# Performance work log

Hardware: AMD Instinct MI355X
Metric: run time of the kernel (lower is better)

Reference implementation:

```python
import jax, jax.numpy as jnp
import numpy as np

KSIZE, SCALE, STRIDE, SOFTMAX_SCALE = 3, 3, 1, 10.0
ESCAPE_NAN = 1e-4
DN = ('NCHW', 'OIHW', 'NCHW')


def same_pad(x, k, stride):
    # torch same_padding: pad so out = ceil(in/stride)
    H, W = x.shape[-2], x.shape[-1]
    oh, ow = -(-H // stride), -(-W // stride)
    ph = max(0, (oh - 1) * stride + k - H)
    pw = max(0, (ow - 1) * stride + k - W)
    return jnp.pad(x, ((0, 0), (0, 0), (ph // 2, ph - ph // 2), (pw // 2, pw - pw // 2)))


def extract_patches(img, k, stride):
    # img [B,C,H,W] already padded -> [B, L, C, k, k], matching torch Unfold ordering (C slowest, kh, kw)
    B, C, H, W = img.shape
    oh, ow = (H - k) // stride + 1, (W - k) // stride + 1
    cols = [img[:, :, i:i + stride * oh:stride, j:j + stride * ow:stride]
            for i in range(k) for j in range(k)]
    p = jnp.stack(cols, axis=2)                      # [B, C, k*k, oh, ow]
    p = p.reshape(B, C, k, k, oh * ow)               # [B, C, k, k, L]
    return jnp.transpose(p, (0, 4, 1, 2, 3))         # [B, L, C, k, k]


def conv1x1_prelu(x, W, b, a):
    y = jnp.einsum('bchw,oc->bohw', x, W) + b[None, :, None, None]
    return jnp.where(y >= 0, y, a * y)


def bilinear_down(x, Ho, Wo):
    # F.interpolate(mode='bilinear', align_corners=False), no antialias
    H, W = x.shape[-2], x.shape[-1]
    def coords(o, s):
        src = (jnp.arange(o, dtype=jnp.float32) + 0.5) * (s / o) - 0.5
        src = jnp.clip(src, 0.0, s - 1.0)
        i0 = jnp.floor(src).astype(jnp.int32)
        i1 = jnp.minimum(i0 + 1, s - 1)
        return i0, i1, src - i0.astype(jnp.float32)
    y0, y1, wy = coords(Ho, H)
    x0, x1, wx = coords(Wo, W)
    r = x[:, :, y0, :] * (1.0 - wy)[:, None] + x[:, :, y1, :] * wy[:, None]
    return r[:, :, :, x0] * (1.0 - wx) + r[:, :, :, x1] * wx


def forward(x, Wa, ba, aa, Wm1, bm1, am1, Wm2, bm2, am2):
    B, C, H, W = x.shape
    kernel = SCALE * KSIZE  # 9
    embed_w = conv1x1_prelu(x, Wa, ba, aa)      # [B,C,H,W]
    match = conv1x1_prelu(x, Wm1, bm1, am1)     # [B,C/2,H,W]
    # large-scale patches used as conv_transpose kernels: [B, L, C, 9, 9]
    raw_w = extract_patches(same_pad(embed_w, kernel, STRIDE * SCALE), kernel, STRIDE * SCALE)
    Hr, Wr = H // SCALE, W // SCALE
    ref = conv1x1_prelu(bilinear_down(x, Hr, Wr), Wm2, bm2, am2)  # [B,C/2,Hr,Wr]
    # small-scale patches used as correlation kernels: [B, L, C/2, 3, 3]
    w = extract_patches(same_pad(ref, KSIZE, STRIDE), KSIZE, STRIDE)
    norm = jnp.sqrt(jnp.sum(w * w, axis=(2, 3, 4), keepdims=True))
    wn = w / jnp.maximum(norm, ESCAPE_NAN)
    xp = same_pad(match, KSIZE, 1)  # [B,C/2,H+2,W+2]

    def corr(xi, wi):  # xi [C/2,H+2,W+2], wi [L,C/2,3,3] -> [L,H,W]
        return jax.lax.conv_general_dilated(xi[None], wi, (1, 1), 'VALID', dimension_numbers=DN)[0]

    y = jax.vmap(corr)(xp, wn)                  # [B,L,H,W]
    y = jax.nn.softmax(y * SOFTMAX_SCALE, axis=1)

    pad = kernel - 1 - SCALE  # conv_transpose2d(stride=3, padding=3) equivalent padding = 5

    def tconv(yi, rwi):  # yi [L,H,W], rwi [L,C,9,9] -> [C,3H,3W]
        k = jnp.transpose(jnp.flip(rwi, (-2, -1)), (1, 0, 2, 3))  # [C,L,9,9]
        return jax.lax.conv_general_dilated(
            yi[None], k, (1, 1), [(pad, pad), (pad, pad)],
            lhs_dilation=(STRIDE * SCALE, STRIDE * SCALE), dimension_numbers=DN)[0]

    out = jax.vmap(tconv)(y, raw_w) / 6.0       # [B,C,3H,3W]
    return out


def setup_inputs() -> dict:
    key = jax.random.key(0)
    ks = jax.random.split(key, 8)
    B, C, H, W = 4, 64, 60, 60
    C2 = C // 2
    return {
        'x': jax.random.normal(ks[0], (B, C, H, W), jnp.float32),
        'Wa': jax.random.normal(ks[1], (C, C), jnp.float32) * 0.1,
        'ba': jax.random.normal(ks[2], (C,), jnp.float32) * 0.1,
        'aa': jnp.full((1,), 0.25, jnp.float32),
        'Wm1': jax.random.normal(ks[3], (C2, C), jnp.float32) * 0.1,
        'bm1': jax.random.normal(ks[4], (C2,), jnp.float32) * 0.1,
        'am1': jnp.full((1,), 0.25, jnp.float32),
        'Wm2': jax.random.normal(ks[5], (C2, C), jnp.float32) * 0.1,
        'bm2': jax.random.normal(ks[6], (C2,), jnp.float32) * 0.1,
        'am2': jnp.full((1,), 0.25, jnp.float32),
    }


def reference(x, Wa, ba, aa, Wm1, bm1, am1, Wm2, bm2, am2):
    return forward(x, Wa, ba, aa, Wm1, bm1, am1, Wm2, bm2, am2)
```

## Files before the change

### kernel.cpp

```cpp
#include <hip/hip_runtime.h>
#include <hip/hip_bf16.h>

typedef __hip_bfloat16 bf16_t;
using f32x4  = __attribute__((ext_vector_type(4))) float;
using bf16x8 = __attribute__((ext_vector_type(8))) short;

#define NB 4
#define NC 64
#define NC2 32
#define NH 60
#define NW 60
#define NPIX (NH*NW)
#define HP 66
#define MP 62
#define HR 20
#define RP 22
#define NL 400
#define OHW 180
#define KPAD 512

#define OFF_XPB   2230272
#define OFF_REFP  3214336
#define OFF_YBL   3462144
#define OFF_AP    14982144
#define OFF_EB    29727744
#define OFF_XP    32087040
#define OFF_RF    40381440

__global__ __launch_bounds__(256) void k_conv(
    const float* __restrict__ x,
    const float* __restrict__ Wa,  const float* __restrict__ ba,  const float* __restrict__ aa,
    const float* __restrict__ Wm1, const float* __restrict__ bm1, const float* __restrict__ am1,
    const float* __restrict__ Wm2, const float* __restrict__ bm2, const float* __restrict__ am2,
    bf16_t* __restrict__ E_bt, bf16_t* __restrict__ xpb, float* __restrict__ refp) {
  int bid = blockIdx.x;
  int t = threadIdx.x;
  if (bid < 300) {
    __shared__ float Ws[64*64];
    __shared__ float bs[64];
    __shared__ float al;
    int b = bid / 75, pblk = bid % 75;
    for (int i = t; i < 64*64; i += 256) {
      int co = i >> 6, c = i & 63;
      Ws[c*64 + co] = Wa[i];
    }
    if (t < 64) bs[t] = ba[t];
    if (t == 0) al = aa[0];
    __syncthreads();
    int lane = t & 63, wid = t >> 6;
    int pix0 = pblk*48 + wid*12;
    const float* xb = x + b*NC*NPIX + pix0;
    float acc[12];
    #pragma unroll
    for (int p = 0; p < 12; ++p) acc[p] = bs[lane];
    for (int c = 0; c < 64; ++c) {
      float wv = Ws[c*64 + lane];
      const float* xc = xb + c*NPIX;
      #pragma unroll
      for (int p = 0; p < 12; ++p)
        acc[p] = fmaf(xc[p], wv, acc[p]);
    }
    #pragma unroll
    for (int p = 0; p < 12; ++p) {
      float v = acc[p];
      v = v >= 0.f ? v : al*v;
      int pix = pix0 + p;
      int ph = pix / NW, pw = pix % NW;
      E_bt[((b*HP + ph+3)*HP + (pw+3))*NC + lane] = __float2bfloat16(v);
    }
  } else if (bid < 2100) {
    int idx = (bid - 300)*256 + t;
    int pix = idx % NPIX; int tmp = idx / NPIX;
    int co = tmp % NC2; int b = tmp / NC2;
    float alpha = am1[0];
    const float* xb = x + b*NC*NPIX + pix;
    const float* wr = Wm1 + co*64;
    float acc = bm1[co];
    #pragma unroll 8
    for (int c = 0; c < 64; ++c)
      acc = fmaf(xb[c*NPIX], wr[c], acc);
    acc = acc >= 0.f ? acc : alpha*acc;
    int ph = pix / NW, pw = pix % NW;
    xpb[((b*NC2 + co)*MP + ph+1)*MP + (pw+1)] = __float2bfloat16(acc);
  } else {
    int idx = (bid - 2100)*256 + t;
    int pos = idx % (HR*HR); int tmp = idx / (HR*HR);
    int co = tmp % NC2; int b = tmp / NC2;
    int hr = pos / HR, wr_ = pos % HR;
    float alpha = am2[0];
    const float* xb = x + b*NC*NPIX + (3*hr+1)*NW + (3*wr_+1);
    const float* wrow = Wm2 + co*64;
    float acc = bm2[co];
    #pragma unroll 8
    for (int c = 0; c < 64; ++c)
      acc = fmaf(xb[c*NPIX], wrow[c], acc);
    acc = acc >= 0.f ? acc : alpha*acc;
    refp[((b*NC2 + co)*RP + hr+1)*RP + (wr_+1)] = acc;
  }
}

__global__ __launch_bounds__(256) void k_swz(
    const bf16_t* __restrict__ xpb, const float* __restrict__ refp,
    const bf16_t* __restrict__ E_bt,
    bf16_t* __restrict__ Xp, bf16_t* __restrict__ Rf, bf16_t* __restrict__ Eb) {
  __shared__ float scl[16];
  int bid = blockIdx.x;
  int t = threadIdx.x;
  if (bid < 2025) {
    int tid = bid*256 + t;
    int slot = tid & 63; int rest = tid >> 6;
    int ks = rest % 9; int rest2 = rest / 9;
    int mblk = rest2 % 225; int b = rest2 / 225;
    int m = mblk*16 + (slot & 15);
    int h = m / NW, w = m % NW;
    int k0 = ks*32 + (slot >> 4)*8;
    const bf16_t* xb = xpb + (size_t)b*NC2*MP*MP;
    union { bf16_t a[8]; bf16x8 v; } u;
    #pragma unroll
    for (int j = 0; j < 8; ++j) {
      int k = k0 + j;
      int c = k / 9, r = k % 9;
      int i = r / 3, j2 = r % 3;
      u.a[j] = xb[(c*MP + h + i)*MP + w + j2];
    }
    *(bf16x8*)(Xp + (size_t)tid*8) = u.v;
  } else if (bid < 2125) {
    int r2 = bid - 2025;
    int nblk = r2 % 25, b = r2 / 25;
    int ll = t >> 4, sub = t & 15;
    int l = nblk*16 + ll;
    int lh = l / HR, lw = l % HR;
    const float* rb = refp + (size_t)b*NC2*RP*RP;
    float ss = 0.f;
    #pragma unroll
    for (int e0 = 0; e0 < 18; ++e0) {
      int e = sub*18 + e0;
      int c = e / 9, r = e % 9;
      int i = r / 3, j = r % 3;
      float v = rb[(c*RP + lh + i)*RP + lw + j];
      ss = fmaf(v, v, ss);
    }
    #pragma unroll
    for (int off = 1; off < 16; off <<= 1)
      ss += __shfl_xor(ss, off);
    if (sub == 0) scl[ll] = 10.f / fmaxf(sqrtf(ss), 1e-4f);
    __syncthreads();
    for (int sidx = t; sidx < 576; sidx += 256) {
      int ks = sidx >> 6, slot = sidx & 63;
      int l2 = nblk*16 + (slot & 15);
      int lh2 = l2 / HR, lw2 = l2 % HR;
      float sc = scl[slot & 15];
      int k0 = ks*32 + (slot >> 4)*8;
      union { bf16_t a[8]; bf16x8 v; } u;
      #pragma unroll
      for (int j = 0; j < 8; ++j) {
        int k = k0 + j;
        int c = k / 9, r = k % 9;
        int i = r / 3, j2 = r % 3;
        u.a[j] = __float2bfloat16(rb[(c*RP + lh2 + i)*RP + lw2 + j2] * sc);
      }
      *(bf16x8*)(Rf + ((size_t)(b*25 + nblk)*576 + sidx)*8) = u.v;
    }
  } else {
    int r2 = bid - 2125;
    int n = r2 % 576, b = r2 / 576;
    int c = n / 9, n9 = n % 9, rr = n9 / 3, s = n9 % 3;
    size_t nbase = ((size_t)(b*12 + n/48)*16);
    const unsigned short* Eu = (const unsigned short*)E_bt;
    unsigned short* Ebu = (unsigned short*)Eb;
    for (int k = t; k < KPAD; k += 256) {
      unsigned short v = 0;
      if (k < 484) {
        int u = k / 22, vv = k % 22;
        v = Eu[((size_t)((b*HP + 3*u + rr)*HP + 3*vv + s))*NC + c];
      }
      size_t idx = (((nbase + (k>>5))*3 + (n%48)/16)*64 + ((k>>3)&3)*16 + (n&15))*8 + (k&7);
      Ebu[idx] = v;
    }
  }
}

__global__ __launch_bounds__(64) void k_cgemm(
    const bf16x8* __restrict__ Xp, const bf16x8* __restrict__ Rf,
    bf16_t* __restrict__ y_bl) {
  __shared__ __align__(16) bf16_t ytile[48][80];
  int L = threadIdx.x;
  int o = blockIdx.x;
  int xcd = o & 7, sl = o >> 3;
  int w = (xcd < 4 ? xcd*188 : 752 + (xcd-4)*187) + sl;
  int b = w / 375; int rem = w % 375;
  int mt = rem / 5, nt = rem % 5;
  const bf16x8* pa = Xp + ((size_t)(b*225 + mt*3)*9)*64 + L;
  const bf16x8* pb = Rf + ((size_t)(b*25 + nt*5)*9)*64 + L;
  f32x4 acc[3][5];
  #pragma unroll
  for (int i = 0; i < 3; ++i)
    #pragma unroll
    for (int j = 0; j < 5; ++j)
      acc[i][j] = {0.f, 0.f, 0.f, 0.f};
  bf16x8 af[3], bf[5], afn[3], bfn[5];
  #pragma unroll
  for (int i = 0; i < 3; ++i) af[i] = pa[i*576];
  #pragma unroll
  for (int j = 0; j < 5; ++j) bf[j] = pb[j*576];
  for (int ks = 0; ks < 9; ++ks) {
    if (ks < 8) {
      #pragma unroll
      for (int i = 0; i < 3; ++i) afn[i] = pa[i*576 + (ks+1)*64];
      #pragma unroll
      for (int j = 0; j < 5; ++j) bfn[j] = pb[j*576 + (ks+1)*64];
    }
    #pragma unroll
    for (int i = 0; i < 3; ++i)
      #pragma unroll
      for (int j = 0; j < 5; ++j)
        acc[i][j] = __builtin_amdgcn_mfma_f32_16x16x32_bf16(af[i], bf[j], acc[i][j], 0, 0, 0);
    #pragma unroll
    for (int i = 0; i < 3; ++i) af[i] = afn[i];
    #pragma unroll
    for (int j = 0; j < 5; ++j) bf[j] = bfn[j];
  }
  int quad = L >> 4, col = L & 15;
  #pragma unroll
  for (int mf = 0; mf < 3; ++mf)
    #pragma unroll
    for (int r = 0; r < 4; ++r)
      #pragma unroll
      for (int nf = 0; nf < 5; ++nf)
        ytile[mf*16 + quad*4 + r][nf*16 + col] = __float2bfloat16(acc[mf][nf][r]);
  __syncthreads();
  bf16_t* dst0 = y_bl + ((size_t)(b*NPIX + mt*48))*NL + nt*80;
  for (int i = L; i < 480; i += 64) {
    int row = i / 10, seg = i % 10;
    *(bf16x8*)(dst0 + (size_t)row*NL + seg*8) = *(const bf16x8*)&ytile[row][seg*8];
  }
}

__device__ __forceinline__ float lo_bf(unsigned int u) {
  return __uint_as_float(u << 16);
}
__device__ __forceinline__ float hi_bf(unsigned int u) {
  return __uint_as_float(u & 0xffff0000u);
}
__device__ __forceinline__ float u16_bf(unsigned short u) {
  return __uint_as_float(((unsigned int)u) << 16);
}
__device__ __forceinline__ unsigned short bf_bits(float f) {
  union { bf16_t h; unsigned short u; } c;
  c.h = __float2bfloat16(f);
  return c.u;
}

__global__ __launch_bounds__(512) void k_saprime(
    const unsigned int* __restrict__ y_b32, bf16_t* __restrict__ Ap) {
  __shared__ uint4 raw[2592];
  unsigned short* ysp = (unsigned short*)raw;
  int t = threadIdx.x;
  int b = blockIdx.z;
  int h0base = blockIdx.y*4, w0base = blockIdx.x*4;
  for (int i = t; i < 2592; i += 512) raw[i] = uint4{0,0,0,0};
  __syncthreads();

  int wave = t >> 6, lane = t & 63;
  bool act = lane < 50;
  for (int pos = wave; pos < 36; pos += 8) {
    int i = pos / 6, jj = pos % 6;
    int hh = h0base - 1 + i, ww = w0base - 1 + jj;
    if (!((unsigned)hh < NH && (unsigned)ww < NW)) continue;
    const uint4* src4 = (const uint4*)(y_b32 + ((size_t)(b*NPIX + hh*NW + ww))*200);
    uint4 v = act ? src4[lane] : uint4{0,0,0,0};
    float f[8];
    if (act) {
      f[0] = lo_bf(v.x); f[1] = hi_bf(v.x);
      f[2] = lo_bf(v.y); f[3] = hi_bf(v.y);
      f[4] = lo_bf(v.z); f[5] = hi_bf(v.z);
      f[6] = lo_bf(v.w); f[7] = hi_bf(v.w);
    } else {
      #pragma unroll
      for (int k = 0; k < 8; ++k) f[k] = -1e30f;
    }
    float m = -1e30f;
    #pragma unroll
    for (int k = 0; k < 8; ++k) m = fmaxf(m, f[k]);
    #pragma unroll
    for (int off = 32; off > 0; off >>= 1)
      m = fmaxf(m, __shfl_xor(m, off));
    float s = 0.f;
    #pragma unroll
    for (int k = 0; k < 8; ++k) {
      float e = __expf(f[k] - m);
      f[k] = e;
      s += e;
    }
    #pragma unroll
    for (int off = 32; off > 0; off >>= 1)
      s += __shfl_xor(s, off);
    float r = 1.f / s;
    if (act) {
      #pragma unroll
      for (int k = 0; k < 4; ++k) {
        int l2 = lane*4 + k;
        int lh = l2 / 10, lw = 2*l2 - 20*lh;
        union { bf16_t h[2]; unsigned int u; } pk;
        pk.h[0] = __float2bfloat16(f[2*k]   * r);
        pk.h[1] = __float2bfloat16(f[2*k+1] * r);
        *(unsigned int*)&ysp[pos*576 + (lh+2)*24 + (lw+2)] = pk.u;
      }
    }
  }
  __syncthreads();

  int row = t >> 5;
  int klane = t & 31;
  int h0r = row >> 2, w0r = row & 3;
  int m = (h0base + h0r)*NW + (w0base + w0r);
  int pblk = m / 80, pf = (m % 80) >> 4, mrow = m & 15;
  size_t rowbase = ((size_t)(b*45 + pblk)*16);
  const unsigned short* basep = ysp + (h0r*6 + w0r)*576;
  unsigned short* Apu = (unsigned short*)Ap;
  for (int kk = 0; kk < 8; ++kk) {
    int k = kk*64 + 2*klane;
    float a0 = 0.f, a1 = 0.f;
    if (k < 484) {
      int u = k / 22, v = k - 22*u;
      const unsigned short* q = basep + u*24 + v;
      #pragma unroll
      for (int dh = 0; dh < 3; ++dh) {
        unsigned int p0 = *(const unsigned int*)(q + dh*3480);
        a0 += lo_bf(p0); a1 += hi_bf(p0);
        a0 += u16_bf(q[dh*3480 + 577]);
        a1 += u16_bf(q[dh*3480 + 578]);
        unsigned int p2 = *(const unsigned int*)(q + dh*3480 + 1154);
        a0 += lo_bf(p2); a1 += hi_bf(p2);
      }
    }
    unsigned int pk = ((unsigned int)bf_bits(a1) << 16) | bf_bits(a0);
    size_t idx = (((rowbase + (k>>5))*5 + pf)*64 + ((k>>3)&3)*16 + mrow)*8 + (k&7);
    *(unsigned int*)&Apu[idx] = pk;
  }
}

__global__ __launch_bounds__(64) void k_tgemm(
    const bf16x8* __restrict__ Eb, const bf16x8* __restrict__ Ap,
    float* __restrict__ out) {
  __shared__ __align__(16) float otile[80][52];
  int L = threadIdx.x;
  int o = blockIdx.x;
  int w = (o & 7)*270 + (o >> 3);
  int b = w / 540; int rem = w % 540;
  int pbi = rem / 12, rb = rem % 12;
  const bf16x8* pa = Eb + ((size_t)(b*12 + rb)*16)*3*64 + L;
  const bf16x8* pp = Ap + ((size_t)(b*45 + pbi)*16)*5*64 + L;
  f32x4 acc[3][5];
  #pragma unroll
  for (int i = 0; i < 3; ++i)
    #pragma unroll
    for (int j = 0; j < 5; ++j)
      acc[i][j] = {0.f, 0.f, 0.f, 0.f};
  bf16x8 af[3], bf[5], afn[3], bfn[5];
  #pragma unroll
  for (int i = 0; i < 3; ++i) af[i] = pa[i*64];
  #pragma unroll
  for (int j = 0; j < 5; ++j) bf[j] = pp[j*64];
  for (int ks = 0; ks < 16; ++ks) {
    if (ks < 15) {
      const bf16x8* na = pa + (ks+1)*192;
      const bf16x8* nb = pp + (ks+1)*320;
      #pragma unroll
      for (int i = 0; i < 3; ++i) afn[i] = na[i*64];
      #pragma unroll
      for (int j = 0; j < 5; ++j) bfn[j] = nb[j*64];
    }
    #pragma unroll
    for (int i = 0; i < 3; ++i)
      #pragma unroll
      for (int j = 0; j < 5; ++j)
        acc[i][j] = __builtin_amdgcn_mfma_f32_16x16x32_bf16(af[i], bf[j], acc[i][j], 0, 0, 0);
    #pragma unroll
    for (int i = 0; i < 3; ++i) af[i] = afn[i];
    #pragma unroll
    for (int j = 0; j < 5; ++j) bf[j] = bfn[j];
  }
  int quad = L >> 4, col = L & 15;
  const float sc = 1.f/6.f;
  #pragma unroll
  for (int pf = 0; pf < 5; ++pf)
    #pragma unroll
    for (int rf = 0; rf < 3; ++rf) {
      f32x4 v = acc[rf][pf];
      v[0] *= sc; v[1] *= sc; v[2] *= sc; v[3] *= sc;
      *(f32x4*)&otile[pf*16 + col][rf*16 + quad*4] = v;
    }
  __syncthreads();
  float* ob = out + b*(NC*OHW*OHW);
  int m0 = pbi*80;
  for (int i = L; i < 960; i += 64) {
    int p = i / 60, q = i % 60;
    int nl = rb*48 + p*3;
    int c = nl / 9, rr = (nl % 9) / 3;
    int f0 = q*4;
    f32x4 v;
    #pragma unroll
    for (int j = 0; j < 4; ++j) {
      int f = f0 + j;
      int mi = f / 3, s = f - 3*mi;
      v[j] = otile[mi][p*3 + s];
    }
    int mi0 = f0 / 3, s0 = f0 % 3;
    int m = m0 + mi0;
    int h0 = m / 60, w0 = m % 60;
    *(f32x4*)&ob[c*32400 + (3*h0 + rr)*180 + 3*w0 + s0] = v;
  }
}

extern "C" void kernel_launch(void* const* d_in, const int* in_sizes, int n_in,
                              void* d_out, int out_size, void* d_ws, size_t ws_size,
                              hipStream_t stream) {
  (void)in_sizes; (void)n_in; (void)out_size; (void)ws_size;
  const float* x   = (const float*)d_in[0];
  const float* Wa  = (const float*)d_in[1];
  const float* ba  = (const float*)d_in[2];
  const float* aa  = (const float*)d_in[3];
  const float* Wm1 = (const float*)d_in[4];
  const float* bm1 = (const float*)d_in[5];
  const float* am1 = (const float*)d_in[6];
  const float* Wm2 = (const float*)d_in[7];
  const float* bm2 = (const float*)d_in[8];
  const float* am2 = (const float*)d_in[9];
  float* out = (float*)d_out;

  char* base = (char*)d_ws;
  bf16_t* E_bt  = (bf16_t*)base;
  bf16_t* xpb   = (bf16_t*)(base + OFF_XPB);
  float*  refp  = (float*)(base + OFF_REFP);
  bf16_t* y_bl  = (bf16_t*)(base + OFF_YBL);
  bf16_t* ApSwz = (bf16_t*)(base + OFF_AP);
  bf16_t* EbSwz = (bf16_t*)(base + OFF_EB);
  bf16_t* XpSwz = (bf16_t*)(base + OFF_XP);
  bf16_t* RfSwz = (bf16_t*)(base + OFF_RF);

  hipMemsetAsync(d_ws, 0, (size_t)OFF_YBL, stream);

  k_conv<<<2300, 256, 0, stream>>>(x, Wa, ba, aa, Wm1, bm1, am1, Wm2, bm2, am2,
                                   E_bt, xpb, refp);
  k_swz<<<4429, 256, 0, stream>>>(xpb, refp, E_bt, XpSwz, RfSwz, EbSwz);
  k_cgemm<<<1500, 64, 0, stream>>>((const bf16x8*)XpSwz, (const bf16x8*)RfSwz, y_bl);
  k_saprime<<<dim3(15, 15, NB), 512, 0, stream>>>((const unsigned int*)y_bl, ApSwz);
  k_tgemm<<<2160, 64, 0, stream>>>((const bf16x8*)EbSwz, (const bf16x8*)ApSwz, out);
}
```

Baseline: 166.1 us.

## Fuse softmax into correlation GEMM epilogue with full-row blocks

```diff
diff --git a/kernel.cpp b/kernel.cpp
--- a/kernel.cpp
+++ b/kernel.cpp
@@ -180,62 +180,6 @@
   }
 }
 
-__global__ __launch_bounds__(64) void k_cgemm(
-    const bf16x8* __restrict__ Xp, const bf16x8* __restrict__ Rf,
-    bf16_t* __restrict__ y_bl) {
-  __shared__ __align__(16) bf16_t ytile[48][80];
-  int L = threadIdx.x;
-  int o = blockIdx.x;
-  int xcd = o & 7, sl = o >> 3;
-  int w = (xcd < 4 ? xcd*188 : 752 + (xcd-4)*187) + sl;
-  int b = w / 375; int rem = w % 375;
-  int mt = rem / 5, nt = rem % 5;
-  const bf16x8* pa = Xp + ((size_t)(b*225 + mt*3)*9)*64 + L;
-  const bf16x8* pb = Rf + ((size_t)(b*25 + nt*5)*9)*64 + L;
-  f32x4 acc[3][5];
-  #pragma unroll
-  for (int i = 0; i < 3; ++i)
-    #pragma unroll
-    for (int j = 0; j < 5; ++j)
-      acc[i][j] = {0.f, 0.f, 0.f, 0.f};
-  bf16x8 af[3], bf[5], afn[3], bfn[5];
-  #pragma unroll
-  for (int i = 0; i < 3; ++i) af[i] = pa[i*576];
-  #pragma unroll
-  for (int j = 0; j < 5; ++j) bf[j] = pb[j*576];
-  for (int ks = 0; ks < 9; ++ks) {
-    if (ks < 8) {
-      #pragma unroll
-      for (int i = 0; i < 3; ++i) afn[i] = pa[i*576 + (ks+1)*64];
-      #pragma unroll
-      for (int j = 0; j < 5; ++j) bfn[j] = pb[j*576 + (ks+1)*64];
-    }
-    #pragma unroll
-    for (int i = 0; i < 3; ++i)
-      #pragma unroll
-      for (int j = 0; j < 5; ++j)
-        acc[i][j] = __builtin_amdgcn_mfma_f32_16x16x32_bf16(af[i], bf[j], acc[i][j], 0, 0, 0);
-    #pragma unroll
-    for (int i = 0; i < 3; ++i) af[i] = afn[i];
-    #pragma unroll
-    for (int j = 0; j < 5; ++j) bf[j] = bfn[j];
-  }
-  int quad = L >> 4, col = L & 15;
-  #pragma unroll
-  for (int mf = 0; mf < 3; ++mf)
-    #pragma unroll
-    for (int r = 0; r < 4; ++r)
-      #pragma unroll
-      for (int nf = 0; nf < 5; ++nf)
-        ytile[mf*16 + quad*4 + r][nf*16 + col] = __float2bfloat16(acc[mf][nf][r]);
-  __syncthreads();
-  bf16_t* dst0 = y_bl + ((size_t)(b*NPIX + mt*48))*NL + nt*80;
-  for (int i = L; i < 480; i += 64) {
-    int row = i / 10, seg = i % 10;
-    *(bf16x8*)(dst0 + (size_t)row*NL + seg*8) = *(const bf16x8*)&ytile[row][seg*8];
-  }
-}
-
 __device__ __forceinline__ float lo_bf(unsigned int u) {
   return __uint_as_float(u << 16);
 }
@@ -249,6 +193,99 @@
   union { bf16_t h; unsigned short u; } c;
   c.h = __float2bfloat16(f);
   return c.u;
+}
+
+__global__ __launch_bounds__(320) void k_cgemm(
+    const bf16x8* __restrict__ Xp, const bf16x8* __restrict__ Rf,
+    bf16_t* __restrict__ y_bl) {
+  __shared__ __align__(16) bf16_t ytile[48][408];
+  int t = threadIdx.x;
+  int L = t & 63, nt = t >> 6;
+  int o = blockIdx.x;
+  int xcd = o & 7, sl = o >> 3;
+  int w = (xcd < 4 ? xcd*38 : 152 + (xcd-4)*37) + sl;
+  int b = w / 75, mt = w % 75;
+  const bf16x8* pa = Xp + ((size_t)(b*225 + mt*3)*9)*64 + L;
+  const bf16x8* pb = Rf + ((size_t)(b*25 + nt*5)*9)*64 + L;
+  f32x4 acc[3][5];
+  #pragma unroll
+  for (int i = 0; i < 3; ++i)
+    #pragma unroll
+    for (int j = 0; j < 5; ++j)
+      acc[i][j] = {0.f, 0.f, 0.f, 0.f};
+  bf16x8 af[3], bf[5], afn[3], bfn[5];
+  #pragma unroll
+  for (int i = 0; i < 3; ++i) af[i] = pa[i*576];
+  #pragma unroll
+  for (int j = 0; j < 5; ++j) bf[j] = pb[j*576];
+  for (int ks = 0; ks < 9; ++ks) {
+    if (ks < 8) {
+      #pragma unroll
+      for (int i = 0; i < 3; ++i) afn[i] = pa[i*576 + (ks+1)*64];
+      #pragma unroll
+      for (int j = 0; j < 5; ++j) bfn[j] = pb[j*576 + (ks+1)*64];
+    }
+    #pragma unroll
+    for (int i = 0; i < 3; ++i)
+      #pragma unroll
+      for (int j = 0; j < 5; ++j)
+        acc[i][j] = __builtin_amdgcn_mfma_f32_16x16x32_bf16(af[i], bf[j], acc[i][j], 0, 0, 0);
+    #pragma unroll
+    for (int i = 0; i < 3; ++i) af[i] = afn[i];
+    #pragma unroll
+    for (int j = 0; j < 5; ++j) bf[j] = bfn[j];
+  }
+  int quad = L >> 4, col = L & 15;
+  #pragma unroll
+  for (int mf = 0; mf < 3; ++mf)
+    #pragma unroll
+    for (int r = 0; r < 4; ++r)
+      #pragma unroll
+      for (int nf = 0; nf < 5; ++nf)
+        ytile[mf*16 + quad*4 + r][nt*80 + nf*16 + col] = __float2bfloat16(acc[mf][nf][r]);
+  __syncthreads();
+
+  bool act = L < 50;
+  for (int row = nt; row < 48; row += 5) {
+    uint4 v = act ? *(const uint4*)&ytile[row][L*8] : uint4{0u,0u,0u,0u};
+    float f[8];
+    if (act) {
+      f[0] = lo_bf(v.x); f[1] = hi_bf(v.x);
+      f[2] = lo_bf(v.y); f[3] = hi_bf(v.y);
+      f[4] = lo_bf(v.z); f[5] = hi_bf(v.z);
+      f[6] = lo_bf(v.w); f[7] = hi_bf(v.w);
+    } else {
+      #pragma unroll
+      for (int k = 0; k < 8; ++k) f[k] = -1e30f;
+    }
+    float m = -1e30f;
+    #pragma unroll
+    for (int k = 0; k < 8; ++k) m = fmaxf(m, f[k]);
+    #pragma unroll
+    for (int off = 32; off > 0; off >>= 1)
+      m = fmaxf(m, __shfl_xor(m, off));
+    float s = 0.f;
+    #pragma unroll
+    for (int k = 0; k < 8; ++k) {
+      float e = __expf(f[k] - m);
+      f[k] = e;
+      s += e;
+    }
+    #pragma unroll
+    for (int off = 32; off > 0; off >>= 1)
+      s += __shfl_xor(s, off);
+    float r = 1.f / s;
+    if (act) {
+      union { bf16_t h[2]; unsigned int u; } p0, p1, p2, p3;
+      p0.h[0] = __float2bfloat16(f[0]*r); p0.h[1] = __float2bfloat16(f[1]*r);
+      p1.h[0] = __float2bfloat16(f[2]*r); p1.h[1] = __float2bfloat16(f[3]*r);
+      p2.h[0] = __float2bfloat16(f[4]*r); p2.h[1] = __float2bfloat16(f[5]*r);
+      p3.h[0] = __float2bfloat16(f[6]*r); p3.h[1] = __float2bfloat16(f[7]*r);
+      uint4 pr = uint4{p0.u, p1.u, p2.u, p3.u};
+      bf16_t* rowp = y_bl + ((size_t)(b*NPIX + mt*48 + row))*NL;
+      *(uint4*)(rowp + L*8) = pr;
+    }
+  }
 }
 
 __global__ __launch_bounds__(512) void k_saprime(
@@ -267,45 +304,15 @@
     int i = pos / 6, jj = pos % 6;
     int hh = h0base - 1 + i, ww = w0base - 1 + jj;
     if (!((unsigned)hh < NH && (unsigned)ww < NW)) continue;
+    if (!act) continue;
     const uint4* src4 = (const uint4*)(y_b32 + ((size_t)(b*NPIX + hh*NW + ww))*200);
-    uint4 v = act ? src4[lane] : uint4{0,0,0,0};
-    float f[8];
-    if (act) {
-      f[0] = lo_bf(v.x); f[1] = hi_bf(v.x);
-      f[2] = lo_bf(v.y); f[3] = hi_bf(v.y);
-      f[4] = lo_bf(v.z); f[5] = hi_bf(v.z);
-      f[6] = lo_bf(v.w); f[7] = hi_bf(v.w);
-    } else {
-      #pragma unroll
-      for (int k = 0; k < 8; ++k) f[k] = -1e30f;
-    }
-    float m = -1e30f;
-    #pragma unroll
-    for (int k = 0; k < 8; ++k) m = fmaxf(m, f[k]);
-    #pragma unroll
-    for (int off = 32; off > 0; off >>= 1)
-      m = fmaxf(m, __shfl_xor(m, off));
-    float s = 0.f;
-    #pragma unroll
-    for (int k = 0; k < 8; ++k) {
-      float e = __expf(f[k] - m);
-      f[k] = e;
-      s += e;
-    }
-    #pragma unroll
-    for (int off = 32; off > 0; off >>= 1)
-      s += __shfl_xor(s, off);
-    float r = 1.f / s;
-    if (act) {
-      #pragma unroll
-      for (int k = 0; k < 4; ++k) {
-        int l2 = lane*4 + k;
-        int lh = l2 / 10, lw = 2*l2 - 20*lh;
-        union { bf16_t h[2]; unsigned int u; } pk;
-        pk.h[0] = __float2bfloat16(f[2*k]   * r);
-        pk.h[1] = __float2bfloat16(f[2*k+1] * r);
-        *(unsigned int*)&ysp[pos*576 + (lh+2)*24 + (lw+2)] = pk.u;
-      }
+    uint4 v = src4[lane];
+    unsigned int wsv[4] = {v.x, v.y, v.z, v.w};
+    #pragma unroll
+    for (int k = 0; k < 4; ++k) {
+      int l2 = lane*4 + k;
+      int lh = l2 / 10, lw = 2*l2 - 20*lh;
+      *(unsigned int*)&ysp[pos*576 + (lh+2)*24 + (lw+2)] = wsv[k];
     }
   }
   __syncthreads();
@@ -444,7 +451,7 @@
   k_conv<<<2300, 256, 0, stream>>>(x, Wa, ba, aa, Wm1, bm1, am1, Wm2, bm2, am2,
                                    E_bt, xpb, refp);
   k_swz<<<4429, 256, 0, stream>>>(xpb, refp, E_bt, XpSwz, RfSwz, EbSwz);
-  k_cgemm<<<1500, 64, 0, stream>>>((const bf16x8*)XpSwz, (const bf16x8*)RfSwz, y_bl);
+  k_cgemm<<<300, 320, 0, stream>>>((const bf16x8*)XpSwz, (const bf16x8*)RfSwz, y_bl);
   k_saprime<<<dim3(15, 15, NB), 512, 0, stream>>>((const unsigned int*)y_bl, ApSwz);
   k_tgemm<<<2160, 64, 0, stream>>>((const bf16x8*)EbSwz, (const bf16x8*)ApSwz, out);
 }
```

Measured after the change: 177.7 us. +7.0%, slower.
